# Kernel tuning notes

Hardware: AMD Instinct MI355X
Metric: run time of the kernel (lower is better)

Reference implementation:

```python
import jax, jax.numpy as jnp
import numpy as np

N_NODES = 100000
N_EDGES = 3200000
N_FEAT = 128
N_GRAPHS = 64


def setup_inputs() -> dict:
    key = jax.random.key(0)
    ks = jax.random.split(key, 8)
    x = jax.random.normal(ks[0], (N_NODES, N_FEAT), dtype=jnp.float32)
    edge_index = jax.random.randint(ks[1], (2, N_EDGES), 0, N_NODES, dtype=jnp.int64)
    batch = jnp.sort(jax.random.randint(ks[2], (N_NODES,), 0, N_GRAPHS, dtype=jnp.int64))
    # GCNConv weights (glorot-style scale) and biases
    W1 = jax.random.normal(ks[3], (N_FEAT, 32), dtype=jnp.float32) / np.sqrt(N_FEAT)
    b1 = jnp.zeros((32,), dtype=jnp.float32)
    W2 = jax.random.normal(ks[4], (32, 16), dtype=jnp.float32) / np.sqrt(32.0)
    b2 = jnp.zeros((16,), dtype=jnp.float32)
    lin_w = jax.random.normal(ks[5], (16, 1), dtype=jnp.float32) / np.sqrt(16.0)
    lin_b = jnp.zeros((1,), dtype=jnp.float32)
    return {"x": x, "edge_index": edge_index, "batch": batch,
            "W1": W1, "b1": b1, "W2": W2, "b2": b2,
            "lin_w": lin_w, "lin_b": lin_b}


def _gcn_conv(x, W, b, src, dst, deg_inv_sqrt, n_nodes):
    # transform first (fewer features downstream when out_dim < in_dim)
    xw = x @ W  # [N, out]
    norm = deg_inv_sqrt[src] * deg_inv_sqrt[dst]  # [E+N]
    msg = xw[src] * norm[:, None]  # gather + scale
    out = jax.ops.segment_sum(msg, dst, num_segments=n_nodes)  # scatter-add
    return out + b


def reference(x, edge_index, batch, W1, b1, W2, b2, lin_w, lin_b):
    n_nodes = x.shape[0]
    self_loop = jnp.arange(n_nodes, dtype=edge_index.dtype)
    src = jnp.concatenate([edge_index[0], self_loop])
    dst = jnp.concatenate([edge_index[1], self_loop])
    # symmetric GCN normalization with self-loops
    deg = jax.ops.segment_sum(jnp.ones_like(src, dtype=x.dtype), dst,
                              num_segments=n_nodes)
    deg_inv_sqrt = jnp.where(deg > 0, jax.lax.rsqrt(jnp.maximum(deg, 1.0)), 0.0)

    h = _gcn_conv(x, W1, b1, src, dst, deg_inv_sqrt, n_nodes)
    h = jax.nn.relu(h)
    # F.dropout with training=False (eval) is identity
    h = _gcn_conv(h, W2, b2, src, dst, deg_inv_sqrt, n_nodes)

    # global_mean_pool over batch index
    sums = jax.ops.segment_sum(h, batch, num_segments=N_GRAPHS)  # [G,16]
    cnts = jax.ops.segment_sum(jnp.ones((n_nodes,), dtype=h.dtype), batch,
                               num_segments=N_GRAPHS)
    pooled = sums / jnp.maximum(cnts, 1.0)[:, None]
    return pooled @ lin_w + lin_b  # [G,1]
```

## Files before the change

kernel.cpp:

```cpp
#include <hip/hip_runtime.h>

#define NN 100000
#define NE 3200000
#define NF 128
#define C1 32
#define C2 16
#define NG 64
#define BKT_SH 7
#define BKT_W  128
#define NBKT   782
#define CH     8192
#define NW     391
#define RSTR   784
#define MAPCAP 6400

#define OFF_BCNT  0
#define OFF_BST   1024
#define OFF_RUN   2048
#define OFF_ROW   308608
#define OFF_DIS   408624
#define OFF_POOL  508624
#define OFF_CNTF  509648
#define OFF_EDG   509712
#define OFF_XS1H0 OFF_EDG
#define OFF_XS1H1 (OFF_EDG + NN*8)
#define OFF_H1A   (OFF_EDG + NE)
#define OFF_H1B   (OFF_H1A + NN*16)
#define OFF_XS2B  (OFF_H1B + NN*16)
#define OFF_COL   (OFF_XS2B + NN*8)

__device__ __forceinline__ unsigned pack_bf2(float a, float b) {
    unsigned ua = __float_as_uint(a);
    unsigned ub = __float_as_uint(b);
    ua = (ua + 0x7fffu + ((ua >> 16) & 1u)) >> 16;
    ub = (ub + 0x7fffu + ((ub >> 16) & 1u)) & 0xffff0000u;
    return ua | ub;
}
__device__ __forceinline__ float2 unpack_bf2(unsigned u) {
    return make_float2(__uint_as_float(u << 16), __uint_as_float(u & 0xffff0000u));
}

__global__ __launch_bounds__(256) void k_part(
    const int* __restrict__ S, const int* __restrict__ D,
    unsigned* __restrict__ edgebuf, int* __restrict__ runstart,
    int* __restrict__ bcnt)
{
    __shared__ int lhist[1024];
    __shared__ int lstart[1024];
    __shared__ int lcur[NBKT];
    __shared__ int sd[256];
    __shared__ unsigned lsort[CH];
    const int w = blockIdx.x;
    const int t = threadIdx.x;
    const int e0 = w * CH;
    const int n = min(CH, NE - e0);

    for (int i = t; i < 1024; i += 256) lhist[i] = 0;
    __syncthreads();
    for (int i = t; i < n; i += 256)
        atomicAdd(&lhist[(unsigned)D[e0 + i] >> BKT_SH], 1);
    __syncthreads();
    for (int i = t; i < NBKT; i += 256) atomicAdd(&bcnt[i], lhist[i]);
    int c0 = lhist[t * 4 + 0], c1 = lhist[t * 4 + 1];
    int c2 = lhist[t * 4 + 2], c3 = lhist[t * 4 + 3];
    int ts = c0 + c1 + c2 + c3;
    sd[t] = ts;
    __syncthreads();
    for (int off = 1; off < 256; off <<= 1) {
        int v = (t >= off) ? sd[t - off] : 0;
        __syncthreads();
        sd[t] += v;
        __syncthreads();
    }
    int excl = sd[t] - ts;
    lstart[t * 4 + 0] = excl;
    lstart[t * 4 + 1] = excl + c0;
    lstart[t * 4 + 2] = excl + c0 + c1;
    lstart[t * 4 + 3] = excl + c0 + c1 + c2;
    __syncthreads();
    for (int i = t; i < 783; i += 256) runstart[w * RSTR + i] = lstart[i];
    for (int i = t; i < NBKT; i += 256) lcur[i] = lstart[i];
    __syncthreads();
    for (int i = t; i < n; i += 256) {
        int s = S[e0 + i], d = D[e0 + i];
        int pos = atomicAdd(&lcur[(unsigned)d >> BKT_SH], 1);
        lsort[pos] = ((unsigned)s << BKT_SH) | (unsigned)(d & (BKT_W - 1));
    }
    __syncthreads();
    for (int i = t; i < n; i += 256) edgebuf[e0 + i] = lsort[i];
}

__global__ __launch_bounds__(256) void k_bscan(const int* __restrict__ bcnt,
                                               int* __restrict__ bstart,
                                               int* __restrict__ rowstart) {
    __shared__ int sd[256];
    const int t = threadIdx.x;
    const int base = t * 4;
    int c0 = (base + 0 < NBKT) ? bcnt[base + 0] : 0;
    int c1 = (base + 1 < NBKT) ? bcnt[base + 1] : 0;
    int c2 = (base + 2 < NBKT) ? bcnt[base + 2] : 0;
    int c3 = (base + 3 < NBKT) ? bcnt[base + 3] : 0;
    int ts = c0 + c1 + c2 + c3;
    sd[t] = ts;
    __syncthreads();
    for (int off = 1; off < 256; off <<= 1) {
        int v = (t >= off) ? sd[t - off] : 0;
        __syncthreads();
        sd[t] += v;
        __syncthreads();
    }
    int excl = sd[t] - ts;
    if (base + 0 < 783) bstart[base + 0] = excl;
    if (base + 1 < 783) bstart[base + 1] = excl + c0;
    if (base + 2 < 783) bstart[base + 2] = excl + c0 + c1;
    if (base + 3 < 783) bstart[base + 3] = excl + c0 + c1 + c2;
    if (t == 0) rowstart[NN] = NE;
}

__global__ __launch_bounds__(256) void k_fillfused(
    const unsigned* __restrict__ edgebuf, const int* __restrict__ runstart,
    const int* __restrict__ bstart,
    int* __restrict__ rowstart, float* __restrict__ dis, int* __restrict__ colidx)
{
    __shared__ int rl[NW];
    __shared__ int pfx[NW];
    __shared__ int basea[NW];
    __shared__ unsigned short map[MAPCAP];
    __shared__ int lcnt[BKT_W];
    __shared__ int lcur[BKT_W];
    __shared__ int sd[256];
    const int b = blockIdx.x;
    const int t = threadIdx.x;
    const int bs = bstart[b];
    const int total = bstart[b + 1] - bs;

    for (int w = t; w < NW; w += 256) {
        int s0 = runstart[w * RSTR + b];
        int s1 = runstart[w * RSTR + b + 1];
        basea[w] = s0;
        rl[w] = s1 - s0;
    }
    if (t < BKT_W) lcnt[t] = 0;
    __syncthreads();
    {
        int w0 = t * 2;
        int c0 = (w0 < NW) ? rl[w0] : 0;
        int c1 = (w0 + 1 < NW) ? rl[w0 + 1] : 0;
        int ts = c0 + c1;
        sd[t] = ts;
        __syncthreads();
        for (int off = 1; off < 256; off <<= 1) {
            int v = (t >= off) ? sd[t - off] : 0;
            __syncthreads();
            sd[t] += v;
            __syncthreads();
        }
        int excl = sd[t] - ts;
        if (w0 < NW)     pfx[w0]     = excl;
        if (w0 + 1 < NW) pfx[w0 + 1] = excl + c0;
    }
    __syncthreads();
    for (int w = t; w < NW; w += 256) {
        int p = pfx[w], len = rl[w];
        basea[w] = w * CH + basea[w] - p;
        for (int i = 0; i < len; ++i) map[p + i] = (unsigned short)w;
    }
    __syncthreads();
    for (int j = t; j < total; j += 256) {
        unsigned p = edgebuf[basea[map[j]] + j];
        atomicAdd(&lcnt[p & (BKT_W - 1)], 1);
    }
    __syncthreads();
    if (t < BKT_W) lcur[t] = lcnt[t];
    __syncthreads();
    for (int off = 1; off < BKT_W; off <<= 1) {
        int v = (t < BKT_W && t >= off) ? lcur[t - off] : 0;
        __syncthreads();
        if (t < BKT_W) lcur[t] += v;
        __syncthreads();
    }
    if (t < BKT_W) {
        int excl = lcur[t] - lcnt[t];
        int node = b * BKT_W + t;
        if (node < NN) {
            rowstart[node] = bs + excl;
            dis[node] = rsqrtf((float)lcnt[t] + 1.0f);
        }
        lcur[t] = bs + excl;
    }
    __syncthreads();
    for (int j = t; j < total; j += 256) {
        unsigned p = edgebuf[basea[map[j]] + j];
        int pos = atomicAdd(&lcur[p & (BKT_W - 1)], 1);
        colidx[pos] = (int)(p >> BKT_SH);
    }
}

__global__ __launch_bounds__(256) void k_gemm1(
    const float* __restrict__ x, const float* __restrict__ W1,
    const float* __restrict__ dis,
    unsigned* __restrict__ xs1h0, unsigned* __restrict__ xs1h1)
{
    __shared__ float xls[128 * 33];
    __shared__ float wls[32 * 32];
    const int t = threadIdx.x;
    const int tc = t & 7;
    const int tr = t >> 3;
    const int base = blockIdx.x * 128;

    float a[4][4] = {};

    for (int k0 = 0; k0 < NF; k0 += 32) {
        {
            int i = t * 4;
            int kk = i >> 5, c = i & 31;
            *(float4*)&wls[kk * 32 + c] = *(const float4*)&W1[(k0 + kk) * C1 + c];
        }
        #pragma unroll
        for (int r = 0; r < 4; ++r) {
            int n = (t >> 3) + r * 32;
            int j = (t & 7) * 4;
            int node = base + n;
            float4 v = make_float4(0.f, 0.f, 0.f, 0.f);
            if (node < NN) v = *(const float4*)&x[(long long)node * NF + k0 + j];
            xls[n * 33 + j + 0] = v.x;
            xls[n * 33 + j + 1] = v.y;
            xls[n * 33 + j + 2] = v.z;
            xls[n * 33 + j + 3] = v.w;
        }
        __syncthreads();
        #pragma unroll 8
        for (int kk = 0; kk < 32; ++kk) {
            float4 w = *(const float4*)&wls[kk * 32 + tc * 4];
            #pragma unroll
            for (int i = 0; i < 4; ++i) {
                float xv = xls[(tr * 4 + i) * 33 + kk];
                a[i][0] = fmaf(xv, w.x, a[i][0]);
                a[i][1] = fmaf(xv, w.y, a[i][1]);
                a[i][2] = fmaf(xv, w.z, a[i][2]);
                a[i][3] = fmaf(xv, w.w, a[i][3]);
            }
        }
        __syncthreads();
    }
    #pragma unroll
    for (int i = 0; i < 4; ++i) {
        int node = base + tr * 4 + i;
        if (node < NN) {
            float dv = dis[node];
            uint2 o;
            o.x = pack_bf2(a[i][0] * dv, a[i][1] * dv);
            o.y = pack_bf2(a[i][2] * dv, a[i][3] * dv);
            unsigned* dst = (tc < 4) ? &xs1h0[node * 8 + tc * 2]
                                     : &xs1h1[node * 8 + (tc - 4) * 2];
            *(uint2*)dst = o;
        }
    }
}

template<int HALF>
__global__ __launch_bounds__(256) void k_gather1h(
    const unsigned* __restrict__ xsh, const int* __restrict__ colidx,
    const int* __restrict__ rowstart, const float* __restrict__ dis,
    const float* __restrict__ b1, float* __restrict__ h1h)
{
    const int l = threadIdx.x & 7;
    const int v = blockIdx.x * 32 + (threadIdx.x >> 3);
    if (v >= NN) return;
    const int start = rowstart[v];
    const int num = rowstart[v + 1] - start;
    const int* __restrict__ cp = &colidx[start];

    float2 a0 = unpack_bf2(xsh[v * 8 + l]);
    float2 a1 = make_float2(0.f, 0.f), a2 = a1, a3 = a1;
    int i = 0;
    for (; i + 4 <= num; i += 4) {
        int s0 = cp[i], s1 = cp[i + 1], s2 = cp[i + 2], s3 = cp[i + 3];
        float2 u0 = unpack_bf2(xsh[s0 * 8 + l]);
        float2 u1 = unpack_bf2(xsh[s1 * 8 + l]);
        float2 u2 = unpack_bf2(xsh[s2 * 8 + l]);
        float2 u3 = unpack_bf2(xsh[s3 * 8 + l]);
        a0.x += u0.x; a0.y += u0.y;
        a1.x += u1.x; a1.y += u1.y;
        a2.x += u2.x; a2.y += u2.y;
        a3.x += u3.x; a3.y += u3.y;
    }
    for (; i < num; ++i) {
        float2 u = unpack_bf2(xsh[cp[i] * 8 + l]);
        a0.x += u.x; a0.y += u.y;
    }
    float accx = (a0.x + a1.x) + (a2.x + a3.x);
    float accy = (a0.y + a1.y) + (a2.y + a3.y);
    float dv = dis[v];
    float2 bv = *(const float2*)&b1[HALF * 16 + l * 2];
    float2 o;
    o.x = fmaxf(fmaf(accx, dv, bv.x), 0.f);
    o.y = fmaxf(fmaf(accy, dv, bv.y), 0.f);
    *(float2*)&h1h[v * 16 + l * 2] = o;
}

__global__ __launch_bounds__(256) void k_gemm2(
    const float* __restrict__ h1a, const float* __restrict__ h1b,
    const float* __restrict__ W2,
    const float* __restrict__ dis, unsigned* __restrict__ xs2b)
{
    __shared__ float hls[128 * 33];
    __shared__ float wls[32 * 16];
    const int t = threadIdx.x;
    const int base = blockIdx.x * 128;

    if (t < 128) *(float4*)&wls[t * 4] = *(const float4*)&W2[t * 4];

    #pragma unroll
    for (int r = 0; r < 4; ++r) {
        int n = (t >> 3) + r * 32;
        int j = (t & 7) * 4;
        int node = base + n;
        float4 v = make_float4(0.f, 0.f, 0.f, 0.f);
        if (node < NN) {
            v = (j < 16) ? *(const float4*)&h1a[node * 16 + j]
                         : *(const float4*)&h1b[node * 16 + (j - 16)];
        }
        hls[n * 33 + j + 0] = v.x;
        hls[n * 33 + j + 1] = v.y;
        hls[n * 33 + j + 2] = v.z;
        hls[n * 33 + j + 3] = v.w;
    }
    __syncthreads();

    const int tc = t & 3;
    const int tr = t >> 2;
    float a[2][4] = {};
    #pragma unroll 8
    for (int kk = 0; kk < 32; ++kk) {
        float4 w = *(const float4*)&wls[kk * C2 + tc * 4];
        #pragma unroll
        for (int i = 0; i < 2; ++i) {
            float xv = hls[(tr * 2 + i) * 33 + kk];
            a[i][0] = fmaf(xv, w.x, a[i][0]);
            a[i][1] = fmaf(xv, w.y, a[i][1]);
            a[i][2] = fmaf(xv, w.z, a[i][2]);
            a[i][3] = fmaf(xv, w.w, a[i][3]);
        }
    }
    #pragma unroll
    for (int i = 0; i < 2; ++i) {
        int node = base + tr * 2 + i;
        if (node < NN) {
            float dv = dis[node];
            uint2 o;
            o.x = pack_bf2(a[i][0] * dv, a[i][1] * dv);
            o.y = pack_bf2(a[i][2] * dv, a[i][3] * dv);
            *(uint2*)&xs2b[node * 8 + tc * 2] = o;
        }
    }
}

__global__ __launch_bounds__(256) void k_gather2(
    const unsigned* __restrict__ xs2b, const int* __restrict__ colidx,
    const int* __restrict__ rowstart, const float* __restrict__ dis,
    const float* __restrict__ b2, const int* __restrict__ batch,
    float* __restrict__ pool, float* __restrict__ cntf)
{
    __shared__ float psum[NG * C2];
    __shared__ float cs[NG];
    const int t = threadIdx.x;
    for (int i = t; i < NG * C2; i += 256) psum[i] = 0.f;
    if (t < NG) cs[t] = 0.f;
    __syncthreads();

    const int l = t & 7;
    const int v = blockIdx.x * 32 + (t >> 3);
    if (v < NN) {
        const int start = rowstart[v];
        const int num = rowstart[v + 1] - start;
        const int* __restrict__ cp = &colidx[start];

        float2 a0 = unpack_bf2(xs2b[v * 8 + l]);
        float2 a1 = make_float2(0.f, 0.f), a2 = a1, a3 = a1;
        int i = 0;
        for (; i + 4 <= num; i += 4) {
            int s0 = cp[i], s1 = cp[i + 1], s2 = cp[i + 2], s3 = cp[i + 3];
            float2 u0 = unpack_bf2(xs2b[s0 * 8 + l]);
            float2 u1 = unpack_bf2(xs2b[s1 * 8 + l]);
            float2 u2 = unpack_bf2(xs2b[s2 * 8 + l]);
            float2 u3 = unpack_bf2(xs2b[s3 * 8 + l]);
            a0.x += u0.x; a0.y += u0.y;
            a1.x += u1.x; a1.y += u1.y;
            a2.x += u2.x; a2.y += u2.y;
            a3.x += u3.x; a3.y += u3.y;
        }
        for (; i < num; ++i) {
            float2 u = unpack_bf2(xs2b[cp[i] * 8 + l]);
            a0.x += u.x; a0.y += u.y;
        }
        float accx = (a0.x + a1.x) + (a2.x + a3.x);
        float accy = (a0.y + a1.y) + (a2.y + a3.y);
        float dv = dis[v];
        float2 bv = *(const float2*)&b2[l * 2];
        int g = batch[v];
        atomicAdd(&psum[g * C2 + l * 2],     fmaf(accx, dv, bv.x));
        atomicAdd(&psum[g * C2 + l * 2 + 1], fmaf(accy, dv, bv.y));
        if (l == 0) atomicAdd(&cs[g], 1.0f);
    }
    __syncthreads();
    for (int i = t; i < NG * C2; i += 256)
        if (psum[i] != 0.f) atomicAdd(&pool[i], psum[i]);
    if (t < NG && cs[t] != 0.f) atomicAdd(&cntf[t], cs[t]);
}

__global__ void k_final(const float* __restrict__ pool, const float* __restrict__ cntf,
                        const float* __restrict__ lw, const float* __restrict__ lb,
                        float* __restrict__ out)
{
    int g = threadIdx.x;
    if (g < NG) {
        float c = fmaxf(cntf[g], 1.0f);
        float inv = 1.0f / c;
        float s = lb[0];
        #pragma unroll
        for (int k = 0; k < C2; ++k) s = fmaf(pool[g * C2 + k] * inv, lw[k], s);
        out[g] = s;
    }
}

extern "C" void kernel_launch(void* const* d_in, const int* in_sizes, int n_in,
                              void* d_out, int out_size, void* d_ws, size_t ws_size,
                              hipStream_t stream) {
    const float* x     = (const float*)d_in[0];
    const int*   ei    = (const int*)d_in[1];
    const int*   batch = (const int*)d_in[2];
    const float* W1    = (const float*)d_in[3];
    const float* b1    = (const float*)d_in[4];
    const float* W2    = (const float*)d_in[5];
    const float* b2    = (const float*)d_in[6];
    const float* lw    = (const float*)d_in[7];
    const float* lb    = (const float*)d_in[8];
    float* out = (float*)d_out;

    float*    wsf = (float*)d_ws;
    int*      wsi = (int*)d_ws;
    unsigned* wsu = (unsigned*)d_ws;

    int*      bcnt     = wsi + OFF_BCNT;
    int*      bstart   = wsi + OFF_BST;
    int*      runstart = wsi + OFF_RUN;
    int*      rowstart = wsi + OFF_ROW;
    float*    dis      = wsf + OFF_DIS;
    float*    pool     = wsf + OFF_POOL;
    float*    cntf     = wsf + OFF_CNTF;
    unsigned* edgebuf  = wsu + OFF_EDG;
    unsigned* xs1h0    = wsu + OFF_XS1H0;
    unsigned* xs1h1    = wsu + OFF_XS1H1;
    float*    h1a      = wsf + OFF_H1A;
    float*    h1b      = wsf + OFF_H1B;
    unsigned* xs2b     = wsu + OFF_XS2B;
    int*      colidx   = wsi + OFF_COL;

    const int* S = ei;
    const int* D = ei + NE;

    hipMemsetAsync(bcnt, 0, 1024 * sizeof(int), stream);
    hipMemsetAsync(pool, 0, (NG * C2 + NG) * sizeof(float), stream);

    k_part      <<<NW, 256, 0, stream>>>(S, D, edgebuf, runstart, bcnt);
    k_bscan     <<<1, 256, 0, stream>>>(bcnt, bstart, rowstart);
    k_fillfused <<<NBKT, 256, 0, stream>>>(edgebuf, runstart, bstart, rowstart, dis, colidx);
    k_gemm1     <<<(NN + 127) / 128, 256, 0, stream>>>(x, W1, dis, xs1h0, xs1h1);
    k_gather1h<0><<<(NN + 31) / 32, 256, 0, stream>>>(xs1h0, colidx, rowstart, dis, b1, h1a);
    k_gather1h<1><<<(NN + 31) / 32, 256, 0, stream>>>(xs1h1, colidx, rowstart, dis, b1, h1b);
    k_gemm2     <<<(NN + 127) / 128, 256, 0, stream>>>(h1a, h1b, W2, dis, xs2b);
    k_gather2   <<<(NN + 31) / 32, 256, 0, stream>>>(xs2b, colidx, rowstart, dis, b2, batch, pool, cntf);
    k_final     <<<1, 64, 0, stream>>>(pool, cntf, lw, lb, out);
}
```

Before: 304.0 us.

## Fuse layer-2 GEMM into second gather half, widen per-thread loads, fold bias into final

```diff
diff --git a/kernel.cpp b/kernel.cpp
--- a/kernel.cpp
+++ b/kernel.cpp
@@ -25,8 +25,7 @@
 #define OFF_XS1H0 OFF_EDG
 #define OFF_XS1H1 (OFF_EDG + NN*8)
 #define OFF_H1A   (OFF_EDG + NE)
-#define OFF_H1B   (OFF_H1A + NN*16)
-#define OFF_XS2B  (OFF_H1B + NN*16)
+#define OFF_XS2B  (OFF_H1A + NN*16)
 #define OFF_COL   (OFF_XS2B + NN*8)
 
 __device__ __forceinline__ unsigned pack_bf2(float a, float b) {
@@ -38,6 +37,10 @@
 }
 __device__ __forceinline__ float2 unpack_bf2(unsigned u) {
     return make_float2(__uint_as_float(u << 16), __uint_as_float(u & 0xffff0000u));
+}
+__device__ __forceinline__ void acc4(float4& a, uint2 q) {
+    float2 f0 = unpack_bf2(q.x), f1 = unpack_bf2(q.y);
+    a.x += f0.x; a.y += f0.y; a.z += f1.x; a.w += f1.y;
 }
 
 __global__ __launch_bounds__(256) void k_part(
@@ -262,96 +265,91 @@
 __global__ __launch_bounds__(256) void k_gather1h(
     const unsigned* __restrict__ xsh, const int* __restrict__ colidx,
     const int* __restrict__ rowstart, const float* __restrict__ dis,
-    const float* __restrict__ b1, float* __restrict__ h1h)
-{
-    const int l = threadIdx.x & 7;
-    const int v = blockIdx.x * 32 + (threadIdx.x >> 3);
-    if (v >= NN) return;
-    const int start = rowstart[v];
-    const int num = rowstart[v + 1] - start;
-    const int* __restrict__ cp = &colidx[start];
-
-    float2 a0 = unpack_bf2(xsh[v * 8 + l]);
-    float2 a1 = make_float2(0.f, 0.f), a2 = a1, a3 = a1;
-    int i = 0;
-    for (; i + 4 <= num; i += 4) {
-        int s0 = cp[i], s1 = cp[i + 1], s2 = cp[i + 2], s3 = cp[i + 3];
-        float2 u0 = unpack_bf2(xsh[s0 * 8 + l]);
-        float2 u1 = unpack_bf2(xsh[s1 * 8 + l]);
-        float2 u2 = unpack_bf2(xsh[s2 * 8 + l]);
-        float2 u3 = unpack_bf2(xsh[s3 * 8 + l]);
-        a0.x += u0.x; a0.y += u0.y;
-        a1.x += u1.x; a1.y += u1.y;
-        a2.x += u2.x; a2.y += u2.y;
-        a3.x += u3.x; a3.y += u3.y;
-    }
-    for (; i < num; ++i) {
-        float2 u = unpack_bf2(xsh[cp[i] * 8 + l]);
-        a0.x += u.x; a0.y += u.y;
-    }
-    float accx = (a0.x + a1.x) + (a2.x + a3.x);
-    float accy = (a0.y + a1.y) + (a2.y + a3.y);
-    float dv = dis[v];
-    float2 bv = *(const float2*)&b1[HALF * 16 + l * 2];
-    float2 o;
-    o.x = fmaxf(fmaf(accx, dv, bv.x), 0.f);
-    o.y = fmaxf(fmaf(accy, dv, bv.y), 0.f);
-    *(float2*)&h1h[v * 16 + l * 2] = o;
-}
-
-__global__ __launch_bounds__(256) void k_gemm2(
-    const float* __restrict__ h1a, const float* __restrict__ h1b,
-    const float* __restrict__ W2,
-    const float* __restrict__ dis, unsigned* __restrict__ xs2b)
-{
-    __shared__ float hls[128 * 33];
-    __shared__ float wls[32 * 16];
-    const int t = threadIdx.x;
-    const int base = blockIdx.x * 128;
-
-    if (t < 128) *(float4*)&wls[t * 4] = *(const float4*)&W2[t * 4];
-
-    #pragma unroll
-    for (int r = 0; r < 4; ++r) {
-        int n = (t >> 3) + r * 32;
-        int j = (t & 7) * 4;
-        int node = base + n;
-        float4 v = make_float4(0.f, 0.f, 0.f, 0.f);
-        if (node < NN) {
-            v = (j < 16) ? *(const float4*)&h1a[node * 16 + j]
-                         : *(const float4*)&h1b[node * 16 + (j - 16)];
-        }
-        hls[n * 33 + j + 0] = v.x;
-        hls[n * 33 + j + 1] = v.y;
-        hls[n * 33 + j + 2] = v.z;
-        hls[n * 33 + j + 3] = v.w;
-    }
-    __syncthreads();
-
-    const int tc = t & 3;
-    const int tr = t >> 2;
-    float a[2][4] = {};
-    #pragma unroll 8
-    for (int kk = 0; kk < 32; ++kk) {
-        float4 w = *(const float4*)&wls[kk * C2 + tc * 4];
-        #pragma unroll
-        for (int i = 0; i < 2; ++i) {
-            float xv = hls[(tr * 2 + i) * 33 + kk];
-            a[i][0] = fmaf(xv, w.x, a[i][0]);
-            a[i][1] = fmaf(xv, w.y, a[i][1]);
-            a[i][2] = fmaf(xv, w.z, a[i][2]);
-            a[i][3] = fmaf(xv, w.w, a[i][3]);
-        }
-    }
-    #pragma unroll
-    for (int i = 0; i < 2; ++i) {
-        int node = base + tr * 2 + i;
-        if (node < NN) {
-            float dv = dis[node];
+    const float* __restrict__ b1, float* __restrict__ h1a,
+    const float* __restrict__ W2, unsigned* __restrict__ xs2b)
+{
+    __shared__ float w2s[C1 * C2];
+    __shared__ float hrow[64 * 33];
+    const int t = threadIdx.x;
+    if (HALF == 1 && t < 128) *(float4*)&w2s[t * 4] = *(const float4*)&W2[t * 4];
+    const int l = t & 3;
+    const int n = t >> 2;
+    const int v = blockIdx.x * 64 + n;
+    const bool valid = v < NN;
+
+    float4 acc = make_float4(0.f, 0.f, 0.f, 0.f);
+    float dv = 0.f;
+    if (valid) {
+        const int start = rowstart[v];
+        const int num = rowstart[v + 1] - start;
+        const int* __restrict__ cp = &colidx[start];
+        uint2 u = *(const uint2*)&xsh[v * 8 + l * 2];
+        float4 a0 = make_float4(0.f, 0.f, 0.f, 0.f);
+        acc4(a0, u);
+        float4 a1 = make_float4(0.f, 0.f, 0.f, 0.f), a2 = a1, a3 = a1;
+        int i = 0;
+        for (; i + 8 <= num; i += 8) {
+            int s0 = cp[i], s1 = cp[i+1], s2 = cp[i+2], s3 = cp[i+3];
+            int s4 = cp[i+4], s5 = cp[i+5], s6 = cp[i+6], s7 = cp[i+7];
+            uint2 q0 = *(const uint2*)&xsh[s0 * 8 + l * 2];
+            uint2 q1 = *(const uint2*)&xsh[s1 * 8 + l * 2];
+            uint2 q2 = *(const uint2*)&xsh[s2 * 8 + l * 2];
+            uint2 q3 = *(const uint2*)&xsh[s3 * 8 + l * 2];
+            uint2 q4 = *(const uint2*)&xsh[s4 * 8 + l * 2];
+            uint2 q5 = *(const uint2*)&xsh[s5 * 8 + l * 2];
+            uint2 q6 = *(const uint2*)&xsh[s6 * 8 + l * 2];
+            uint2 q7 = *(const uint2*)&xsh[s7 * 8 + l * 2];
+            acc4(a0, q0); acc4(a1, q1); acc4(a2, q2); acc4(a3, q3);
+            acc4(a0, q4); acc4(a1, q5); acc4(a2, q6); acc4(a3, q7);
+        }
+        for (; i < num; ++i) {
+            uint2 q = *(const uint2*)&xsh[cp[i] * 8 + l * 2];
+            acc4(a0, q);
+        }
+        acc.x = (a0.x + a1.x) + (a2.x + a3.x);
+        acc.y = (a0.y + a1.y) + (a2.y + a3.y);
+        acc.z = (a0.z + a1.z) + (a2.z + a3.z);
+        acc.w = (a0.w + a1.w) + (a2.w + a3.w);
+        dv = dis[v];
+    }
+
+    if (HALF == 0) {
+        if (valid) {
+            float4 o;
+            o.x = fmaxf(fmaf(acc.x, dv, b1[l * 4 + 0]), 0.f);
+            o.y = fmaxf(fmaf(acc.y, dv, b1[l * 4 + 1]), 0.f);
+            o.z = fmaxf(fmaf(acc.z, dv, b1[l * 4 + 2]), 0.f);
+            o.w = fmaxf(fmaf(acc.w, dv, b1[l * 4 + 3]), 0.f);
+            *(float4*)&h1a[v * 16 + l * 4] = o;
+        }
+    } else {
+        if (valid) {
+            float4 hh = *(const float4*)&h1a[v * 16 + l * 4];
+            hrow[n * 33 + l * 4 + 0] = hh.x;
+            hrow[n * 33 + l * 4 + 1] = hh.y;
+            hrow[n * 33 + l * 4 + 2] = hh.z;
+            hrow[n * 33 + l * 4 + 3] = hh.w;
+            hrow[n * 33 + 16 + l * 4 + 0] = fmaxf(fmaf(acc.x, dv, b1[16 + l * 4 + 0]), 0.f);
+            hrow[n * 33 + 16 + l * 4 + 1] = fmaxf(fmaf(acc.y, dv, b1[16 + l * 4 + 1]), 0.f);
+            hrow[n * 33 + 16 + l * 4 + 2] = fmaxf(fmaf(acc.z, dv, b1[16 + l * 4 + 2]), 0.f);
+            hrow[n * 33 + 16 + l * 4 + 3] = fmaxf(fmaf(acc.w, dv, b1[16 + l * 4 + 3]), 0.f);
+        }
+        __syncthreads();
+        if (valid) {
+            const float* hr = &hrow[n * 33];
+            float s0 = 0.f, s1 = 0.f, s2 = 0.f, s3 = 0.f;
+            #pragma unroll
+            for (int k = 0; k < 32; ++k) {
+                float hv = hr[k];
+                s0 = fmaf(hv, w2s[k * C2 + l * 4 + 0], s0);
+                s1 = fmaf(hv, w2s[k * C2 + l * 4 + 1], s1);
+                s2 = fmaf(hv, w2s[k * C2 + l * 4 + 2], s2);
+                s3 = fmaf(hv, w2s[k * C2 + l * 4 + 3], s3);
+            }
             uint2 o;
-            o.x = pack_bf2(a[i][0] * dv, a[i][1] * dv);
-            o.y = pack_bf2(a[i][2] * dv, a[i][3] * dv);
-            *(uint2*)&xs2b[node * 8 + tc * 2] = o;
+            o.x = pack_bf2(s0 * dv, s1 * dv);
+            o.y = pack_bf2(s2 * dv, s3 * dv);
+            *(uint2*)&xs2b[v * 8 + l * 2] = o;
         }
     }
 }
@@ -359,7 +357,7 @@
 __global__ __launch_bounds__(256) void k_gather2(
     const unsigned* __restrict__ xs2b, const int* __restrict__ colidx,
     const int* __restrict__ rowstart, const float* __restrict__ dis,
-    const float* __restrict__ b2, const int* __restrict__ batch,
+    const int* __restrict__ batch,
     float* __restrict__ pool, float* __restrict__ cntf)
 {
     __shared__ float psum[NG * C2];
@@ -369,38 +367,46 @@
     if (t < NG) cs[t] = 0.f;
     __syncthreads();
 
-    const int l = t & 7;
-    const int v = blockIdx.x * 32 + (t >> 3);
+    const int l = t & 3;
+    const int n = t >> 2;
+    const int v = blockIdx.x * 64 + n;
     if (v < NN) {
         const int start = rowstart[v];
         const int num = rowstart[v + 1] - start;
         const int* __restrict__ cp = &colidx[start];
-
-        float2 a0 = unpack_bf2(xs2b[v * 8 + l]);
-        float2 a1 = make_float2(0.f, 0.f), a2 = a1, a3 = a1;
+        uint2 u = *(const uint2*)&xs2b[v * 8 + l * 2];
+        float4 a0 = make_float4(0.f, 0.f, 0.f, 0.f);
+        acc4(a0, u);
+        float4 a1 = make_float4(0.f, 0.f, 0.f, 0.f), a2 = a1, a3 = a1;
         int i = 0;
-        for (; i + 4 <= num; i += 4) {
-            int s0 = cp[i], s1 = cp[i + 1], s2 = cp[i + 2], s3 = cp[i + 3];
-            float2 u0 = unpack_bf2(xs2b[s0 * 8 + l]);
-            float2 u1 = unpack_bf2(xs2b[s1 * 8 + l]);
-            float2 u2 = unpack_bf2(xs2b[s2 * 8 + l]);
-            float2 u3 = unpack_bf2(xs2b[s3 * 8 + l]);
-            a0.x += u0.x; a0.y += u0.y;
-            a1.x += u1.x; a1.y += u1.y;
-            a2.x += u2.x; a2.y += u2.y;
-            a3.x += u3.x; a3.y += u3.y;
+        for (; i + 8 <= num; i += 8) {
+            int s0 = cp[i], s1 = cp[i+1], s2 = cp[i+2], s3 = cp[i+3];
+            int s4 = cp[i+4], s5 = cp[i+5], s6 = cp[i+6], s7 = cp[i+7];
+            uint2 q0 = *(const uint2*)&xs2b[s0 * 8 + l * 2];
+            uint2 q1 = *(const uint2*)&xs2b[s1 * 8 + l * 2];
+            uint2 q2 = *(const uint2*)&xs2b[s2 * 8 + l * 2];
+            uint2 q3 = *(const uint2*)&xs2b[s3 * 8 + l * 2];
+            uint2 q4 = *(const uint2*)&xs2b[s4 * 8 + l * 2];
+            uint2 q5 = *(const uint2*)&xs2b[s5 * 8 + l * 2];
+            uint2 q6 = *(const uint2*)&xs2b[s6 * 8 + l * 2];
+            uint2 q7 = *(const uint2*)&xs2b[s7 * 8 + l * 2];
+            acc4(a0, q0); acc4(a1, q1); acc4(a2, q2); acc4(a3, q3);
+            acc4(a0, q4); acc4(a1, q5); acc4(a2, q6); acc4(a3, q7);
         }
         for (; i < num; ++i) {
-            float2 u = unpack_bf2(xs2b[cp[i] * 8 + l]);
-            a0.x += u.x; a0.y += u.y;
-        }
-        float accx = (a0.x + a1.x) + (a2.x + a3.x);
-        float accy = (a0.y + a1.y) + (a2.y + a3.y);
+            uint2 q = *(const uint2*)&xs2b[cp[i] * 8 + l * 2];
+            acc4(a0, q);
+        }
+        float ax = (a0.x + a1.x) + (a2.x + a3.x);
+        float ay = (a0.y + a1.y) + (a2.y + a3.y);
+        float az = (a0.z + a1.z) + (a2.z + a3.z);
+        float aw = (a0.w + a1.w) + (a2.w + a3.w);
         float dv = dis[v];
-        float2 bv = *(const float2*)&b2[l * 2];
         int g = batch[v];
-        atomicAdd(&psum[g * C2 + l * 2],     fmaf(accx, dv, bv.x));
-        atomicAdd(&psum[g * C2 + l * 2 + 1], fmaf(accy, dv, bv.y));
+        atomicAdd(&psum[g * C2 + l * 4 + 0], ax * dv);
+        atomicAdd(&psum[g * C2 + l * 4 + 1], ay * dv);
+        atomicAdd(&psum[g * C2 + l * 4 + 2], az * dv);
+        atomicAdd(&psum[g * C2 + l * 4 + 3], aw * dv);
         if (l == 0) atomicAdd(&cs[g], 1.0f);
     }
     __syncthreads();
@@ -410,6 +416,7 @@
 }
 
 __global__ void k_final(const float* __restrict__ pool, const float* __restrict__ cntf,
+                        const float* __restrict__ b2,
                         const float* __restrict__ lw, const float* __restrict__ lb,
                         float* __restrict__ out)
 {
@@ -419,7 +426,10 @@
         float inv = 1.0f / c;
         float s = lb[0];
         #pragma unroll
-        for (int k = 0; k < C2; ++k) s = fmaf(pool[g * C2 + k] * inv, lw[k], s);
+        for (int k = 0; k < C2; ++k) {
+            s = fmaf(b2[k], lw[k], s);
+            s = fmaf(pool[g * C2 + k] * inv, lw[k], s);
+        }
         out[g] = s;
     }
 }
@@ -453,7 +463,6 @@
     unsigned* xs1h0    = wsu + OFF_XS1H0;
     unsigned* xs1h1    = wsu + OFF_XS1H1;
     float*    h1a      = wsf + OFF_H1A;
-    float*    h1b      = wsf + OFF_H1B;
     unsigned* xs2b     = wsu + OFF_XS2B;
     int*      colidx   = wsi + OFF_COL;
 
@@ -463,13 +472,12 @@
     hipMemsetAsync(bcnt, 0, 1024 * sizeof(int), stream);
     hipMemsetAsync(pool, 0, (NG * C2 + NG) * sizeof(float), stream);
 
-    k_part      <<<NW, 256, 0, stream>>>(S, D, edgebuf, runstart, bcnt);
-    k_bscan     <<<1, 256, 0, stream>>>(bcnt, bstart, rowstart);
-    k_fillfused <<<NBKT, 256, 0, stream>>>(edgebuf, runstart, bstart, rowstart, dis, colidx);
-    k_gemm1     <<<(NN + 127) / 128, 256, 0, stream>>>(x, W1, dis, xs1h0, xs1h1);
-    k_gather1h<0><<<(NN + 31) / 32, 256, 0, stream>>>(xs1h0, colidx, rowstart, dis, b1, h1a);
-    k_gather1h<1><<<(NN + 31) / 32, 256, 0, stream>>>(xs1h1, colidx, rowstart, dis, b1, h1b);
-    k_gemm2     <<<(NN + 127) / 128, 256, 0, stream>>>(h1a, h1b, W2, dis, xs2b);
-    k_gather2   <<<(NN + 31) / 32, 256, 0, stream>>>(xs2b, colidx, rowstart, dis, b2, batch, pool, cntf);
-    k_final     <<<1, 64, 0, stream>>>(pool, cntf, lw, lb, out);
-}
+    k_part       <<<NW, 256, 0, stream>>>(S, D, edgebuf, runstart, bcnt);
+    k_bscan      <<<1, 256, 0, stream>>>(bcnt, bstart, rowstart);
+    k_fillfused  <<<NBKT, 256, 0, stream>>>(edgebuf, runstart, bstart, rowstart, dis, colidx);
+    k_gemm1      <<<(NN + 127) / 128, 256, 0, stream>>>(x, W1, dis, xs1h0, xs1h1);
+    k_gather1h<0><<<(NN + 63) / 64, 256, 0, stream>>>(xs1h0, colidx, rowstart, dis, b1, h1a, W2, xs2b);
+    k_gather1h<1><<<(NN + 63) / 64, 256, 0, stream>>>(xs1h1, colidx, rowstart, dis, b1, h1a, W2, xs2b);
+    k_gather2    <<<(NN + 63) / 64, 256, 0, stream>>>(xs2b, colidx, rowstart, dis, batch, pool, cntf);
+    k_final      <<<1, 64, 0, stream>>>(pool, cntf, b2, lw, lb, out);
+}
```

Measured after the change: 280.2 us. 1.08x faster.
